# Performance work log

Measured on AMD Instinct MI355X. Metric: run time of the kernel, lower is better.

Reference implementation:

```python
import jax, jax.numpy as jnp
import numpy as np

K = 32          # init k
E = 0.003       # EMA rate e


def setup_inputs() -> dict:
    key = jax.random.key(0)
    k1, _ = jax.random.split(key)
    features = jax.random.normal(k1, (512, 6, 8192), dtype=jnp.float32)
    threshold = jnp.zeros((1,), dtype=jnp.float32)
    return {"features": features, "threshold": threshold}


def reference(features, threshold):
    batch_size, n_layers, d_features = features.shape
    batch_k = K * batch_size * n_layers
    flat = features.reshape(-1)                      # [B*L*D]
    topk_vals, topk_idxs = jax.lax.top_k(flat, batch_k)
    topk_vals = jax.nn.relu(topk_vals)
    out = jnp.zeros_like(flat).at[topk_idxs].set(topk_vals)
    out = out.reshape(batch_size, n_layers, d_features)
    min_k = jax.lax.stop_gradient(jnp.min(topk_vals))
    new_threshold = (1.0 - E) * threshold + E * min_k
    return out, new_threshold
```

## Files before the change

### kernel.cpp

```cpp
#include <hip/hip_runtime.h>
#include <stdint.h>

#define K_TOTAL   98304u
#define EMA_RATE  0.003f

#define SBINS      16384
#define SBIN_SHIFT 18
#define SAMPLE_VEC 131072
#define STARGET    8192u
#define P2_BINS    4096
#define P2_SHIFT   12
#define CAP2       65536u
#define EQCAP      256

#define MP_BLOCKS  1024
#define MP_THREADS 256
#define NWAVES     4096
#define WCAP       256
#define OCAP       65536u

__device__ __forceinline__ unsigned f2key(float x) {
    unsigned u = __float_as_uint(x);
    return (u & 0x80000000u) ? ~u : (u | 0x80000000u);
}
__device__ __forceinline__ float key2f(unsigned key) {
    unsigned u = (key & 0x80000000u) ? (key & 0x7FFFFFFFu) : ~key;
    return __uint_as_float(u);
}

__global__ __launch_bounds__(256) void sample_hist_kernel(
        const float4* __restrict__ in, unsigned* __restrict__ shist) {
    __shared__ unsigned h[SBINS];
    for (int i = threadIdx.x; i < SBINS; i += 256) h[i] = 0;
    __syncthreads();
    unsigned tid = blockIdx.x * 256 + threadIdx.x;
    unsigned nth = gridDim.x * 256;
    for (unsigned j = tid; j < SAMPLE_VEC; j += nth) {
        float4 v = in[j];
        atomicAdd(&h[f2key(v.x) >> SBIN_SHIFT], 1u);
        atomicAdd(&h[f2key(v.y) >> SBIN_SHIFT], 1u);
        atomicAdd(&h[f2key(v.z) >> SBIN_SHIFT], 1u);
        atomicAdd(&h[f2key(v.w) >> SBIN_SHIFT], 1u);
    }
    __syncthreads();
    for (int i = threadIdx.x; i < SBINS; i += 256) {
        unsigned c = h[i];
        if (c) atomicAdd(&shist[i], c);
    }
}

__global__ __launch_bounds__(1024) void sample_scan_kernel(
        const unsigned* __restrict__ shist, unsigned* __restrict__ res) {
    __shared__ unsigned psum[1024];
    const int T = 1024;
    const int GB = SBINS / T;
    int t = threadIdx.x;
    int hi = SBINS - 1 - t * GB;
    unsigned c[GB];
    #pragma unroll
    for (int j = 0; j < GB; ++j) c[j] = shist[hi - j];
    unsigned s = 0;
    #pragma unroll
    for (int j = 0; j < GB; ++j) s += c[j];
    psum[t] = s;
    __syncthreads();
    for (int off = 1; off < T; off <<= 1) {
        unsigned o = (t >= off) ? psum[t - off] : 0u;
        __syncthreads();
        psum[t] += o;
        __syncthreads();
    }
    unsigned cum = psum[t] - s;
    for (int j = 0; j < GB; ++j) {
        if (cum < STARGET && cum + c[j] >= STARGET) {
            unsigned bin = (unsigned)(hi - j);
            unsigned bb = (bin > 0) ? bin - 1 : 0;
            res[0] = bb << SBIN_SHIFT;
        }
        cum += c[j];
    }
}

__global__ __launch_bounds__(MP_THREADS) void main_pass_kernel(
        const float4* __restrict__ in, float4* __restrict__ out,
        const unsigned* __restrict__ res,
        uint2* __restrict__ wreg, unsigned* __restrict__ wcnt,
        uint2* __restrict__ ovf, unsigned* __restrict__ ocnt, int nvec) {
    unsigned tid  = blockIdx.x * MP_THREADS + threadIdx.x;
    unsigned nth  = gridDim.x * MP_THREADS;
    unsigned gw   = tid >> 6;
    unsigned lane = threadIdx.x & 63u;
    unsigned base = res[0];
    uint2* wb = wreg + (size_t)gw * WCAP;
    unsigned wcount = 0;
    const float4 z4 = make_float4(0.f, 0.f, 0.f, 0.f);
    for (unsigned i = tid; i < (unsigned)nvec; i += nth) {
        float4 v = in[i];
        out[i] = z4;
        unsigned idx = 4u * i;
        float xs[4] = {v.x, v.y, v.z, v.w};
        #pragma unroll
        for (int c = 0; c < 4; ++c) {
            unsigned key = f2key(xs[c]);
            bool pred = key >= base;
            unsigned long long mask = __ballot(pred);
            if (mask) {
                if (pred) {
                    unsigned prefix = __builtin_amdgcn_mbcnt_hi(
                        (unsigned)(mask >> 32),
                        __builtin_amdgcn_mbcnt_lo((unsigned)mask, 0u));
                    unsigned off = wcount + prefix;
                    if (off < WCAP) {
                        wb[off] = make_uint2(key, idx + c);
                    } else {
                        unsigned q = atomicAdd(ocnt, 1u);
                        if (q < OCAP) ovf[q] = make_uint2(key, idx + c);
                    }
                }
                wcount += (unsigned)__popcll(mask);
            }
        }
    }
    if (lane == 0) wcnt[gw] = (wcount < WCAP) ? wcount : WCAP;
}

__global__ __launch_bounds__(256) void cand_hist_kernel(
        const uint2* __restrict__ wreg, const unsigned* __restrict__ wcnt,
        const uint2* __restrict__ ovf, const unsigned* __restrict__ ocnt,
        const unsigned* __restrict__ res, unsigned* __restrict__ ghist) {
    __shared__ unsigned h[P2_BINS];
    for (int i = threadIdx.x; i < P2_BINS; i += 256) h[i] = 0;
    __syncthreads();
    unsigned base = res[0];
    unsigned tid = blockIdx.x * 256 + threadIdx.x;
    unsigned nth = gridDim.x * 256;
    const unsigned NSLOT = NWAVES * WCAP;
    for (unsigned s = tid; s < NSLOT; s += nth) {
        unsigned w = s >> 8, j = s & 255u;
        if (j < wcnt[w]) {
            unsigned g = (wreg[s].x - base) >> P2_SHIFT;
            if (g > P2_BINS - 1) g = P2_BINS - 1;
            atomicAdd(&h[g], 1u);
        }
    }
    unsigned no = min(*ocnt, OCAP);
    for (unsigned s = tid; s < no; s += nth) {
        unsigned g = (ovf[s].x - base) >> P2_SHIFT;
        if (g > P2_BINS - 1) g = P2_BINS - 1;
        atomicAdd(&h[g], 1u);
    }
    __syncthreads();
    for (int i = threadIdx.x; i < P2_BINS; i += 256) {
        unsigned c = h[i];
        if (c) atomicAdd(&ghist[i], c);
    }
}

__global__ __launch_bounds__(1024) void find_g_kernel(
        const unsigned* __restrict__ ghist, unsigned* __restrict__ res2) {
    __shared__ unsigned psum[1024];
    const int T = 1024;
    const int GB = P2_BINS / T;
    int t = threadIdx.x;
    int hi = P2_BINS - 1 - t * GB;
    unsigned c[GB];
    #pragma unroll
    for (int j = 0; j < GB; ++j) c[j] = ghist[hi - j];
    unsigned s = 0;
    #pragma unroll
    for (int j = 0; j < GB; ++j) s += c[j];
    psum[t] = s;
    __syncthreads();
    for (int off = 1; off < T; off <<= 1) {
        unsigned o = (t >= off) ? psum[t - off] : 0u;
        __syncthreads();
        psum[t] += o;
        __syncthreads();
    }
    unsigned cum = psum[t] - s;
    for (int j = 0; j < GB; ++j) {
        if (cum < K_TOTAL && cum + c[j] >= K_TOTAL) {
            res2[0] = (unsigned)(hi - j);
            res2[1] = K_TOTAL - cum;
        }
        cum += c[j];
    }
}

__global__ __launch_bounds__(256) void scatter_kernel(
        const uint2* __restrict__ wreg, const unsigned* __restrict__ wcnt,
        const uint2* __restrict__ ovf, const unsigned* __restrict__ ocnt,
        const unsigned* __restrict__ res, const unsigned* __restrict__ res2,
        unsigned* __restrict__ kval2, unsigned* __restrict__ cidx2,
        unsigned* __restrict__ cnt2, float* __restrict__ out) {
    unsigned base  = res[0];
    unsigned gstar = res2[0];
    unsigned tid = blockIdx.x * 256 + threadIdx.x;
    unsigned nth = gridDim.x * 256;
    const unsigned NSLOT = NWAVES * WCAP;
    for (unsigned s = tid; s < NSLOT; s += nth) {
        unsigned w = s >> 8, j = s & 255u;
        if (j < wcnt[w]) {
            uint2 e = wreg[s];
            unsigned g = (e.x - base) >> P2_SHIFT;
            if (g > P2_BINS - 1) g = P2_BINS - 1;
            if (g > gstar) {
                out[e.y] = fmaxf(key2f(e.x), 0.0f);
            } else if (g == gstar) {
                unsigned p = atomicAdd(cnt2, 1u);
                if (p < CAP2) { kval2[p] = e.x; cidx2[p] = e.y; }
            }
        }
    }
    unsigned no = min(*ocnt, OCAP);
    for (unsigned s = tid; s < no; s += nth) {
        uint2 e = ovf[s];
        unsigned g = (e.x - base) >> P2_SHIFT;
        if (g > P2_BINS - 1) g = P2_BINS - 1;
        if (g > gstar) {
            out[e.y] = fmaxf(key2f(e.x), 0.0f);
        } else if (g == gstar) {
            unsigned p = atomicAdd(cnt2, 1u);
            if (p < CAP2) { kval2[p] = e.x; cidx2[p] = e.y; }
        }
    }
}

__global__ __launch_bounds__(256) void final_kernel(
        const unsigned* __restrict__ kval2, const unsigned* __restrict__ cidx2,
        const unsigned* __restrict__ cnt2,
        const unsigned* __restrict__ res, const unsigned* __restrict__ res2,
        float* __restrict__ out,
        const float* __restrict__ thr_in, float* __restrict__ thr_out) {
    __shared__ unsigned h[1 << P2_SHIFT];
    __shared__ unsigned psum[256];
    __shared__ unsigned eqidx[EQCAP];
    __shared__ unsigned eqcnt;
    __shared__ unsigned sh_low, sh_need3;
    const int NB = 1 << P2_SHIFT;
    int t = threadIdx.x;
    unsigned nc2   = min(*cnt2, CAP2);
    unsigned base3 = res[0] + (res2[0] << P2_SHIFT);
    unsigned need2 = res2[1];

    for (int i = t; i < NB; i += 256) h[i] = 0;
    if (t == 0) eqcnt = 0;
    __syncthreads();
    for (unsigned i = t; i < nc2; i += 256) {
        unsigned low = kval2[i] - base3;
        if (low > (unsigned)(NB - 1)) low = NB - 1;
        atomicAdd(&h[low], 1u);
    }
    __syncthreads();

    const int GB = NB / 256;
    int hi = NB - 1 - t * GB;
    unsigned s = 0;
    for (int j = 0; j < GB; ++j) s += h[hi - j];
    psum[t] = s;
    __syncthreads();
    for (int off = 1; off < 256; off <<= 1) {
        unsigned o = (t >= off) ? psum[t - off] : 0u;
        __syncthreads();
        psum[t] += o;
        __syncthreads();
    }
    unsigned cum = psum[t] - s;
    for (int j = 0; j < GB; ++j) {
        unsigned c = h[hi - j];
        if (cum < need2 && cum + c >= need2) {
            sh_low = (unsigned)(hi - j);
            sh_need3 = need2 - cum;
        }
        cum += c;
    }
    __syncthreads();
    unsigned kth_key = base3 + sh_low;
    unsigned need3   = sh_need3;

    for (unsigned i = t; i < nc2; i += 256) {
        unsigned key = kval2[i];
        if (key > kth_key) {
            out[cidx2[i]] = fmaxf(key2f(key), 0.0f);
        } else if (key == kth_key) {
            unsigned p = atomicAdd(&eqcnt, 1u);
            if (p < EQCAP) eqidx[p] = cidx2[i];
        }
    }
    __syncthreads();

    unsigned ne = min(eqcnt, (unsigned)EQCAP);
    float vv = key2f(kth_key);
    for (unsigned e = t; e < ne; e += 256) {
        unsigned my = eqidx[e];
        unsigned rank = 0;
        for (unsigned f = 0; f < ne; ++f) rank += (eqidx[f] < my) ? 1u : 0u;
        if (rank < need3) out[my] = fmaxf(vv, 0.0f);
    }

    if (t == 0) {
        float mink = fmaxf(vv, 0.0f);
        thr_out[0] = (1.0f - EMA_RATE) * thr_in[0] + EMA_RATE * mink;
    }
}

extern "C" void kernel_launch(void* const* d_in, const int* in_sizes, int n_in,
                              void* d_out, int out_size, void* d_ws, size_t ws_size,
                              hipStream_t stream) {
    const float* feat   = (const float*)d_in[0];
    const float* thr_in = (const float*)d_in[1];
    float* out = (float*)d_out;
    int N    = in_sizes[0];
    int nvec = N / 4;

    uint8_t* w = (uint8_t*)d_ws;
    unsigned* shist = (unsigned*)w;
    unsigned* ghist = (unsigned*)(w + (64 << 10));
    unsigned* ctr   = (unsigned*)(w + (80 << 10));
    unsigned* ocnt  = ctr + 0;
    unsigned* cnt2  = ctr + 1;
    unsigned* res   = ctr + 4;
    unsigned* res2  = ctr + 8;
    unsigned* wcnt  = (unsigned*)(w + (84 << 10));

    uint2*    wreg  = (uint2*)(w + ((size_t)1 << 20));
    uint2*    ovf   = (uint2*)(w + ((size_t)9 << 20));
    unsigned* kval2 = (unsigned*)(w + ((size_t)10 << 20));
    unsigned* cidx2 = (unsigned*)(w + ((size_t)10 << 20) + CAP2 * 4);

    hipMemsetAsync(d_ws, 0, (84 << 10), stream);

    sample_hist_kernel<<<128, 256, 0, stream>>>((const float4*)feat, shist);
    sample_scan_kernel<<<1,  1024, 0, stream>>>(shist, res);
    main_pass_kernel  <<<MP_BLOCKS, MP_THREADS, 0, stream>>>(
        (const float4*)feat, (float4*)out, res, wreg, wcnt, ovf, ocnt, nvec);
    cand_hist_kernel  <<<128, 256, 0, stream>>>(wreg, wcnt, ovf, ocnt, res, ghist);
    find_g_kernel     <<<1,  1024, 0, stream>>>(ghist, res2);
    scatter_kernel    <<<128, 256, 0, stream>>>(wreg, wcnt, ovf, ocnt, res, res2,
                                                kval2, cidx2, cnt2, out);
    final_kernel      <<<1,   256, 0, stream>>>(kval2, cidx2, cnt2, res, res2,
                                                out, thr_in, out + N);
}
```

Before: 242.4 us.

## Fuse all top-k stages into one cooperative kernel with grid syncs

Replaces the memset and seven separate kernel launches with a single cooperative kernel that uses grid.sync between phases. The workspace is zeroed in-kernel, and the candidate histogram is built during the main pass, removing the separate re-read of candidate buffers. The sample is shrunk to fewer bins and elements, and the scatter phase gives each block its own wave region. This cuts launch and inter-kernel gaps but adds grid-wide barrier costs, needs all 1024 blocks co-resident, and uses a coarser sample threshold that could admit more candidates.

After: 785.6 us. 3.24x slower.

```diff
diff --git a/kernel.cpp b/kernel.cpp
--- a/kernel.cpp
+++ b/kernel.cpp
@@ -1,23 +1,28 @@
 #include <hip/hip_runtime.h>
+#include <hip/hip_cooperative_groups.h>
 #include <stdint.h>
+
+namespace cg = cooperative_groups;
 
 #define K_TOTAL   98304u
 #define EMA_RATE  0.003f
 
-#define SBINS      16384
-#define SBIN_SHIFT 18
-#define SAMPLE_VEC 131072
-#define STARGET    8192u
-#define P2_BINS    4096
-#define P2_SHIFT   12
-#define CAP2       65536u
-#define EQCAP      256
-
-#define MP_BLOCKS  1024
-#define MP_THREADS 256
-#define NWAVES     4096
-#define WCAP       256
-#define OCAP       65536u
+#define GRID_BLOCKS   1024
+#define BLOCK_THREADS 256
+#define NWAVES        4096
+#define WCAP          256
+
+#define SBINS         4096
+#define SSHIFT        20
+#define SAMPLE_V4     16384
+#define SAMPLE_BLOCKS 32
+#define STARGET       640u
+
+#define CBINS         4096
+#define CSHIFT        12
+#define CAP2          16384u
+#define OCAP          65536u
+#define EQCAP         256
 
 __device__ __forceinline__ unsigned f2key(float x) {
     unsigned u = __float_as_uint(x);
@@ -28,316 +33,287 @@
     return __uint_as_float(u);
 }
 
-__global__ __launch_bounds__(256) void sample_hist_kernel(
-        const float4* __restrict__ in, unsigned* __restrict__ shist) {
-    __shared__ unsigned h[SBINS];
-    for (int i = threadIdx.x; i < SBINS; i += 256) h[i] = 0;
-    __syncthreads();
-    unsigned tid = blockIdx.x * 256 + threadIdx.x;
-    unsigned nth = gridDim.x * 256;
-    for (unsigned j = tid; j < SAMPLE_VEC; j += nth) {
-        float4 v = in[j];
-        atomicAdd(&h[f2key(v.x) >> SBIN_SHIFT], 1u);
-        atomicAdd(&h[f2key(v.y) >> SBIN_SHIFT], 1u);
-        atomicAdd(&h[f2key(v.z) >> SBIN_SHIFT], 1u);
-        atomicAdd(&h[f2key(v.w) >> SBIN_SHIFT], 1u);
-    }
-    __syncthreads();
-    for (int i = threadIdx.x; i < SBINS; i += 256) {
-        unsigned c = h[i];
-        if (c) atomicAdd(&shist[i], c);
-    }
-}
-
-__global__ __launch_bounds__(1024) void sample_scan_kernel(
-        const unsigned* __restrict__ shist, unsigned* __restrict__ res) {
-    __shared__ unsigned psum[1024];
-    const int T = 1024;
-    const int GB = SBINS / T;
-    int t = threadIdx.x;
-    int hi = SBINS - 1 - t * GB;
-    unsigned c[GB];
-    #pragma unroll
-    for (int j = 0; j < GB; ++j) c[j] = shist[hi - j];
-    unsigned s = 0;
-    #pragma unroll
-    for (int j = 0; j < GB; ++j) s += c[j];
-    psum[t] = s;
-    __syncthreads();
-    for (int off = 1; off < T; off <<= 1) {
-        unsigned o = (t >= off) ? psum[t - off] : 0u;
-        __syncthreads();
-        psum[t] += o;
-        __syncthreads();
-    }
-    unsigned cum = psum[t] - s;
-    for (int j = 0; j < GB; ++j) {
-        if (cum < STARGET && cum + c[j] >= STARGET) {
-            unsigned bin = (unsigned)(hi - j);
-            unsigned bb = (bin > 0) ? bin - 1 : 0;
-            res[0] = bb << SBIN_SHIFT;
-        }
-        cum += c[j];
-    }
-}
-
-__global__ __launch_bounds__(MP_THREADS) void main_pass_kernel(
-        const float4* __restrict__ in, float4* __restrict__ out,
-        const unsigned* __restrict__ res,
-        uint2* __restrict__ wreg, unsigned* __restrict__ wcnt,
-        uint2* __restrict__ ovf, unsigned* __restrict__ ocnt, int nvec) {
-    unsigned tid  = blockIdx.x * MP_THREADS + threadIdx.x;
-    unsigned nth  = gridDim.x * MP_THREADS;
-    unsigned gw   = tid >> 6;
-    unsigned lane = threadIdx.x & 63u;
-    unsigned base = res[0];
-    uint2* wb = wreg + (size_t)gw * WCAP;
-    unsigned wcount = 0;
-    const float4 z4 = make_float4(0.f, 0.f, 0.f, 0.f);
-    for (unsigned i = tid; i < (unsigned)nvec; i += nth) {
-        float4 v = in[i];
-        out[i] = z4;
-        unsigned idx = 4u * i;
-        float xs[4] = {v.x, v.y, v.z, v.w};
-        #pragma unroll
-        for (int c = 0; c < 4; ++c) {
-            unsigned key = f2key(xs[c]);
-            bool pred = key >= base;
-            unsigned long long mask = __ballot(pred);
-            if (mask) {
-                if (pred) {
-                    unsigned prefix = __builtin_amdgcn_mbcnt_hi(
-                        (unsigned)(mask >> 32),
-                        __builtin_amdgcn_mbcnt_lo((unsigned)mask, 0u));
-                    unsigned off = wcount + prefix;
-                    if (off < WCAP) {
-                        wb[off] = make_uint2(key, idx + c);
-                    } else {
-                        unsigned q = atomicAdd(ocnt, 1u);
-                        if (q < OCAP) ovf[q] = make_uint2(key, idx + c);
-                    }
-                }
-                wcount += (unsigned)__popcll(mask);
-            }
-        }
-    }
-    if (lane == 0) wcnt[gw] = (wcount < WCAP) ? wcount : WCAP;
-}
-
-__global__ __launch_bounds__(256) void cand_hist_kernel(
-        const uint2* __restrict__ wreg, const unsigned* __restrict__ wcnt,
-        const uint2* __restrict__ ovf, const unsigned* __restrict__ ocnt,
-        const unsigned* __restrict__ res, unsigned* __restrict__ ghist) {
-    __shared__ unsigned h[P2_BINS];
-    for (int i = threadIdx.x; i < P2_BINS; i += 256) h[i] = 0;
-    __syncthreads();
-    unsigned base = res[0];
-    unsigned tid = blockIdx.x * 256 + threadIdx.x;
-    unsigned nth = gridDim.x * 256;
-    const unsigned NSLOT = NWAVES * WCAP;
-    for (unsigned s = tid; s < NSLOT; s += nth) {
-        unsigned w = s >> 8, j = s & 255u;
-        if (j < wcnt[w]) {
-            unsigned g = (wreg[s].x - base) >> P2_SHIFT;
-            if (g > P2_BINS - 1) g = P2_BINS - 1;
-            atomicAdd(&h[g], 1u);
-        }
-    }
-    unsigned no = min(*ocnt, OCAP);
-    for (unsigned s = tid; s < no; s += nth) {
-        unsigned g = (ovf[s].x - base) >> P2_SHIFT;
-        if (g > P2_BINS - 1) g = P2_BINS - 1;
-        atomicAdd(&h[g], 1u);
-    }
-    __syncthreads();
-    for (int i = threadIdx.x; i < P2_BINS; i += 256) {
-        unsigned c = h[i];
-        if (c) atomicAdd(&ghist[i], c);
-    }
-}
-
-__global__ __launch_bounds__(1024) void find_g_kernel(
-        const unsigned* __restrict__ ghist, unsigned* __restrict__ res2) {
-    __shared__ unsigned psum[1024];
-    const int T = 1024;
-    const int GB = P2_BINS / T;
-    int t = threadIdx.x;
-    int hi = P2_BINS - 1 - t * GB;
-    unsigned c[GB];
-    #pragma unroll
-    for (int j = 0; j < GB; ++j) c[j] = ghist[hi - j];
-    unsigned s = 0;
-    #pragma unroll
-    for (int j = 0; j < GB; ++j) s += c[j];
-    psum[t] = s;
-    __syncthreads();
-    for (int off = 1; off < T; off <<= 1) {
-        unsigned o = (t >= off) ? psum[t - off] : 0u;
-        __syncthreads();
-        psum[t] += o;
-        __syncthreads();
-    }
-    unsigned cum = psum[t] - s;
-    for (int j = 0; j < GB; ++j) {
-        if (cum < K_TOTAL && cum + c[j] >= K_TOTAL) {
-            res2[0] = (unsigned)(hi - j);
-            res2[1] = K_TOTAL - cum;
-        }
-        cum += c[j];
-    }
-}
-
-__global__ __launch_bounds__(256) void scatter_kernel(
-        const uint2* __restrict__ wreg, const unsigned* __restrict__ wcnt,
-        const uint2* __restrict__ ovf, const unsigned* __restrict__ ocnt,
-        const unsigned* __restrict__ res, const unsigned* __restrict__ res2,
+__global__ __launch_bounds__(BLOCK_THREADS) void topk_all(
+        const float4* __restrict__ in, float4* __restrict__ out4,
+        float* __restrict__ out,
+        unsigned* __restrict__ shist, unsigned* __restrict__ ghist,
+        unsigned* __restrict__ ctrs,  unsigned* __restrict__ wcnt,
+        uint2* __restrict__ wreg,     uint2* __restrict__ ovf,
         unsigned* __restrict__ kval2, unsigned* __restrict__ cidx2,
-        unsigned* __restrict__ cnt2, float* __restrict__ out) {
-    unsigned base  = res[0];
-    unsigned gstar = res2[0];
-    unsigned tid = blockIdx.x * 256 + threadIdx.x;
-    unsigned nth = gridDim.x * 256;
-    const unsigned NSLOT = NWAVES * WCAP;
-    for (unsigned s = tid; s < NSLOT; s += nth) {
-        unsigned w = s >> 8, j = s & 255u;
-        if (j < wcnt[w]) {
-            uint2 e = wreg[s];
-            unsigned g = (e.x - base) >> P2_SHIFT;
-            if (g > P2_BINS - 1) g = P2_BINS - 1;
-            if (g > gstar) {
-                out[e.y] = fmaxf(key2f(e.x), 0.0f);
-            } else if (g == gstar) {
-                unsigned p = atomicAdd(cnt2, 1u);
-                if (p < CAP2) { kval2[p] = e.x; cidx2[p] = e.y; }
-            }
-        }
-    }
-    unsigned no = min(*ocnt, OCAP);
-    for (unsigned s = tid; s < no; s += nth) {
-        uint2 e = ovf[s];
-        unsigned g = (e.x - base) >> P2_SHIFT;
-        if (g > P2_BINS - 1) g = P2_BINS - 1;
-        if (g > gstar) {
-            out[e.y] = fmaxf(key2f(e.x), 0.0f);
-        } else if (g == gstar) {
-            unsigned p = atomicAdd(cnt2, 1u);
-            if (p < CAP2) { kval2[p] = e.x; cidx2[p] = e.y; }
-        }
-    }
-}
-
-__global__ __launch_bounds__(256) void final_kernel(
-        const unsigned* __restrict__ kval2, const unsigned* __restrict__ cidx2,
-        const unsigned* __restrict__ cnt2,
-        const unsigned* __restrict__ res, const unsigned* __restrict__ res2,
-        float* __restrict__ out,
-        const float* __restrict__ thr_in, float* __restrict__ thr_out) {
-    __shared__ unsigned h[1 << P2_SHIFT];
-    __shared__ unsigned psum[256];
+        const float* __restrict__ thr_in, int nvec)
+{
+    cg::grid_group grid = cg::this_grid();
+    __shared__ unsigned h[CBINS];
+    __shared__ unsigned psum[BLOCK_THREADS];
     __shared__ unsigned eqidx[EQCAP];
     __shared__ unsigned eqcnt;
     __shared__ unsigned sh_low, sh_need3;
-    const int NB = 1 << P2_SHIFT;
-    int t = threadIdx.x;
-    unsigned nc2   = min(*cnt2, CAP2);
-    unsigned base3 = res[0] + (res2[0] << P2_SHIFT);
-    unsigned need2 = res2[1];
-
-    for (int i = t; i < NB; i += 256) h[i] = 0;
-    if (t == 0) eqcnt = 0;
-    __syncthreads();
-    for (unsigned i = t; i < nc2; i += 256) {
-        unsigned low = kval2[i] - base3;
-        if (low > (unsigned)(NB - 1)) low = NB - 1;
-        atomicAdd(&h[low], 1u);
-    }
-    __syncthreads();
-
-    const int GB = NB / 256;
-    int hi = NB - 1 - t * GB;
-    unsigned s = 0;
-    for (int j = 0; j < GB; ++j) s += h[hi - j];
-    psum[t] = s;
-    __syncthreads();
-    for (int off = 1; off < 256; off <<= 1) {
-        unsigned o = (t >= off) ? psum[t - off] : 0u;
-        __syncthreads();
-        psum[t] += o;
-        __syncthreads();
-    }
-    unsigned cum = psum[t] - s;
-    for (int j = 0; j < GB; ++j) {
-        unsigned c = h[hi - j];
-        if (cum < need2 && cum + c >= need2) {
-            sh_low = (unsigned)(hi - j);
-            sh_need3 = need2 - cum;
-        }
-        cum += c;
-    }
-    __syncthreads();
-    unsigned kth_key = base3 + sh_low;
-    unsigned need3   = sh_need3;
-
-    for (unsigned i = t; i < nc2; i += 256) {
-        unsigned key = kval2[i];
-        if (key > kth_key) {
-            out[cidx2[i]] = fmaxf(key2f(key), 0.0f);
-        } else if (key == kth_key) {
-            unsigned p = atomicAdd(&eqcnt, 1u);
-            if (p < EQCAP) eqidx[p] = cidx2[i];
-        }
-    }
-    __syncthreads();
-
-    unsigned ne = min(eqcnt, (unsigned)EQCAP);
-    float vv = key2f(kth_key);
-    for (unsigned e = t; e < ne; e += 256) {
-        unsigned my = eqidx[e];
-        unsigned rank = 0;
-        for (unsigned f = 0; f < ne; ++f) rank += (eqidx[f] < my) ? 1u : 0u;
-        if (rank < need3) out[my] = fmaxf(vv, 0.0f);
-    }
-
-    if (t == 0) {
-        float mink = fmaxf(vv, 0.0f);
-        thr_out[0] = (1.0f - EMA_RATE) * thr_in[0] + EMA_RATE * mink;
+
+    const unsigned t    = threadIdx.x;
+    const unsigned gtid = blockIdx.x * BLOCK_THREADS + t;
+
+    if (gtid < SBINS)                   shist[gtid] = 0;
+    else if (gtid < 2 * SBINS)          ghist[gtid - SBINS] = 0;
+    else if (gtid < 2 * SBINS + 8)      ctrs[gtid - 2 * SBINS] = 0;
+    grid.sync();
+
+    if (blockIdx.x < SAMPLE_BLOCKS) {
+        for (int i = t; i < SBINS; i += BLOCK_THREADS) h[i] = 0;
+        __syncthreads();
+        unsigned s0 = blockIdx.x * 512 + t;
+        #pragma unroll
+        for (int u = 0; u < 2; ++u) {
+            float4 v = in[s0 + u * 256];
+            atomicAdd(&h[f2key(v.x) >> SSHIFT], 1u);
+            atomicAdd(&h[f2key(v.y) >> SSHIFT], 1u);
+            atomicAdd(&h[f2key(v.z) >> SSHIFT], 1u);
+            atomicAdd(&h[f2key(v.w) >> SSHIFT], 1u);
+        }
+        __syncthreads();
+        for (int i = t; i < SBINS; i += BLOCK_THREADS) {
+            unsigned c = h[i];
+            if (c) atomicAdd(&shist[i], c);
+        }
+    }
+    grid.sync();
+
+    if (blockIdx.x == 0) {
+        const int GB = SBINS / BLOCK_THREADS;
+        int hi = SBINS - 1 - t * GB;
+        unsigned c[GB];
+        #pragma unroll
+        for (int j = 0; j < GB; ++j) c[j] = shist[hi - j];
+        unsigned s = 0;
+        #pragma unroll
+        for (int j = 0; j < GB; ++j) s += c[j];
+        psum[t] = s;
+        __syncthreads();
+        for (int off = 1; off < BLOCK_THREADS; off <<= 1) {
+            unsigned o = (t >= off) ? psum[t - off] : 0u;
+            __syncthreads();
+            psum[t] += o;
+            __syncthreads();
+        }
+        unsigned cum = psum[t] - s;
+        for (int j = 0; j < GB; ++j) {
+            if (cum < STARGET && cum + c[j] >= STARGET) {
+                unsigned bin = (unsigned)(hi - j);
+                unsigned bb = (bin > 0) ? bin - 1 : 0;
+                ctrs[2] = bb << SSHIFT;
+            }
+            cum += c[j];
+        }
+    }
+    grid.sync();
+
+    {
+        for (int i = t; i < CBINS; i += BLOCK_THREADS) h[i] = 0;
+        __syncthreads();
+        unsigned base = ctrs[2];
+        unsigned nth  = GRID_BLOCKS * BLOCK_THREADS;
+        unsigned gw   = gtid >> 6;
+        unsigned lane = t & 63u;
+        uint2* wb = wreg + (size_t)gw * WCAP;
+        unsigned wcount = 0;
+        const float4 z4 = make_float4(0.f, 0.f, 0.f, 0.f);
+        for (unsigned i = gtid; i < (unsigned)nvec; i += nth) {
+            float4 v = in[i];
+            out4[i] = z4;
+            unsigned idx = 4u * i;
+            float xs[4] = {v.x, v.y, v.z, v.w};
+            #pragma unroll
+            for (int c = 0; c < 4; ++c) {
+                unsigned key = f2key(xs[c]);
+                bool pred = key >= base;
+                unsigned long long mask = __ballot(pred);
+                if (mask) {
+                    if (pred) {
+                        unsigned prefix = __builtin_amdgcn_mbcnt_hi(
+                            (unsigned)(mask >> 32),
+                            __builtin_amdgcn_mbcnt_lo((unsigned)mask, 0u));
+                        unsigned off = wcount + prefix;
+                        unsigned g = (key - base) >> CSHIFT;
+                        if (g > CBINS - 1) g = CBINS - 1;
+                        atomicAdd(&h[g], 1u);
+                        if (off < WCAP) {
+                            wb[off] = make_uint2(key, idx + c);
+                        } else {
+                            unsigned q = atomicAdd(&ctrs[0], 1u);
+                            if (q < OCAP) ovf[q] = make_uint2(key, idx + c);
+                        }
+                    }
+                    wcount += (unsigned)__popcll(mask);
+                }
+            }
+        }
+        if (lane == 0) wcnt[gw] = (wcount < WCAP) ? wcount : WCAP;
+        __syncthreads();
+        for (int i = t; i < CBINS; i += BLOCK_THREADS) {
+            unsigned c = h[i];
+            if (c) atomicAdd(&ghist[i], c);
+        }
+    }
+    grid.sync();
+
+    if (blockIdx.x == 0) {
+        const int GB = CBINS / BLOCK_THREADS;
+        int hi = CBINS - 1 - t * GB;
+        unsigned c[GB];
+        #pragma unroll
+        for (int j = 0; j < GB; ++j) c[j] = ghist[hi - j];
+        unsigned s = 0;
+        #pragma unroll
+        for (int j = 0; j < GB; ++j) s += c[j];
+        psum[t] = s;
+        __syncthreads();
+        for (int off = 1; off < BLOCK_THREADS; off <<= 1) {
+            unsigned o = (t >= off) ? psum[t - off] : 0u;
+            __syncthreads();
+            psum[t] += o;
+            __syncthreads();
+        }
+        unsigned cum = psum[t] - s;
+        for (int j = 0; j < GB; ++j) {
+            if (cum < K_TOTAL && cum + c[j] >= K_TOTAL) {
+                ctrs[3] = (unsigned)(hi - j);
+                ctrs[4] = K_TOTAL - cum;
+            }
+            cum += c[j];
+        }
+    }
+    grid.sync();
+
+    {
+        unsigned base  = ctrs[2];
+        unsigned gstar = ctrs[3];
+        unsigned slot0 = blockIdx.x * 4 * WCAP;
+        for (unsigned j = t; j < 4 * WCAP; j += BLOCK_THREADS) {
+            unsigned w = (slot0 + j) >> 8;
+            if ((j & 255u) < wcnt[w]) {
+                uint2 e = wreg[slot0 + j];
+                unsigned g = (e.x - base) >> CSHIFT;
+                if (g > CBINS - 1) g = CBINS - 1;
+                if (g > gstar) {
+                    out[e.y] = fmaxf(key2f(e.x), 0.0f);
+                } else if (g == gstar) {
+                    unsigned p = atomicAdd(&ctrs[1], 1u);
+                    if (p < CAP2) { kval2[p] = e.x; cidx2[p] = e.y; }
+                }
+            }
+        }
+        if (blockIdx.x == 0) {
+            unsigned no = min(ctrs[0], (unsigned)OCAP);
+            for (unsigned s = t; s < no; s += BLOCK_THREADS) {
+                uint2 e = ovf[s];
+                unsigned g = (e.x - base) >> CSHIFT;
+                if (g > CBINS - 1) g = CBINS - 1;
+                if (g > gstar) {
+                    out[e.y] = fmaxf(key2f(e.x), 0.0f);
+                } else if (g == gstar) {
+                    unsigned p = atomicAdd(&ctrs[1], 1u);
+                    if (p < CAP2) { kval2[p] = e.x; cidx2[p] = e.y; }
+                }
+            }
+        }
+    }
+    grid.sync();
+
+    if (blockIdx.x == 0) {
+        unsigned nc2   = min(ctrs[1], (unsigned)CAP2);
+        unsigned base3 = ctrs[2] + (ctrs[3] << CSHIFT);
+        unsigned need2 = ctrs[4];
+        const int NB = 1 << CSHIFT;
+
+        for (int i = t; i < NB; i += BLOCK_THREADS) h[i] = 0;
+        if (t == 0) eqcnt = 0;
+        __syncthreads();
+        for (unsigned i = t; i < nc2; i += BLOCK_THREADS) {
+            unsigned low = kval2[i] - base3;
+            if (low > (unsigned)(NB - 1)) low = NB - 1;
+            atomicAdd(&h[low], 1u);
+        }
+        __syncthreads();
+
+        const int GB = NB / BLOCK_THREADS;
+        int hi = NB - 1 - t * GB;
+        unsigned s = 0;
+        for (int j = 0; j < GB; ++j) s += h[hi - j];
+        psum[t] = s;
+        __syncthreads();
+        for (int off = 1; off < BLOCK_THREADS; off <<= 1) {
+            unsigned o = (t >= off) ? psum[t - off] : 0u;
+            __syncthreads();
+            psum[t] += o;
+            __syncthreads();
+        }
+        unsigned cum = psum[t] - s;
+        for (int j = 0; j < GB; ++j) {
+            unsigned c = h[hi - j];
+            if (cum < need2 && cum + c >= need2) {
+                sh_low = (unsigned)(hi - j);
+                sh_need3 = need2 - cum;
+            }
+            cum += c;
+        }
+        __syncthreads();
+        unsigned kth_key = base3 + sh_low;
+        unsigned need3   = sh_need3;
+
+        for (unsigned i = t; i < nc2; i += BLOCK_THREADS) {
+            unsigned key = kval2[i];
+            if (key > kth_key) {
+                out[cidx2[i]] = fmaxf(key2f(key), 0.0f);
+            } else if (key == kth_key) {
+                unsigned p = atomicAdd(&eqcnt, 1u);
+                if (p < EQCAP) eqidx[p] = cidx2[i];
+            }
+        }
+        __syncthreads();
+
+        unsigned ne = min(eqcnt, (unsigned)EQCAP);
+        float vv = key2f(kth_key);
+        for (unsigned e = t; e < ne; e += BLOCK_THREADS) {
+            unsigned my = eqidx[e];
+            unsigned rank = 0;
+            for (unsigned f = 0; f < ne; ++f) rank += (eqidx[f] < my) ? 1u : 0u;
+            if (rank < need3) out[my] = fmaxf(vv, 0.0f);
+        }
+
+        if (t == 0) {
+            float mink = fmaxf(vv, 0.0f);
+            out[4 * (size_t)nvec] =
+                (1.0f - EMA_RATE) * thr_in[0] + EMA_RATE * mink;
+        }
     }
 }
 
 extern "C" void kernel_launch(void* const* d_in, const int* in_sizes, int n_in,
                               void* d_out, int out_size, void* d_ws, size_t ws_size,
                               hipStream_t stream) {
-    const float* feat   = (const float*)d_in[0];
-    const float* thr_in = (const float*)d_in[1];
-    float* out = (float*)d_out;
+    const float4* feat   = (const float4*)d_in[0];
+    const float*  thr_in = (const float*)d_in[1];
+    float*  out  = (float*)d_out;
+    float4* out4 = (float4*)d_out;
     int N    = in_sizes[0];
     int nvec = N / 4;
 
     uint8_t* w = (uint8_t*)d_ws;
     unsigned* shist = (unsigned*)w;
-    unsigned* ghist = (unsigned*)(w + (64 << 10));
-    unsigned* ctr   = (unsigned*)(w + (80 << 10));
-    unsigned* ocnt  = ctr + 0;
-    unsigned* cnt2  = ctr + 1;
-    unsigned* res   = ctr + 4;
-    unsigned* res2  = ctr + 8;
-    unsigned* wcnt  = (unsigned*)(w + (84 << 10));
-
+    unsigned* ghist = (unsigned*)(w + (16 << 10));
+    unsigned* ctrs  = (unsigned*)(w + (32 << 10));
+    unsigned* wcnt  = (unsigned*)(w + (36 << 10));
     uint2*    wreg  = (uint2*)(w + ((size_t)1 << 20));
-    uint2*    ovf   = (uint2*)(w + ((size_t)9 << 20));
-    unsigned* kval2 = (unsigned*)(w + ((size_t)10 << 20));
-    unsigned* cidx2 = (unsigned*)(w + ((size_t)10 << 20) + CAP2 * 4);
-
-    hipMemsetAsync(d_ws, 0, (84 << 10), stream);
-
-    sample_hist_kernel<<<128, 256, 0, stream>>>((const float4*)feat, shist);
-    sample_scan_kernel<<<1,  1024, 0, stream>>>(shist, res);
-    main_pass_kernel  <<<MP_BLOCKS, MP_THREADS, 0, stream>>>(
-        (const float4*)feat, (float4*)out, res, wreg, wcnt, ovf, ocnt, nvec);
-    cand_hist_kernel  <<<128, 256, 0, stream>>>(wreg, wcnt, ovf, ocnt, res, ghist);
-    find_g_kernel     <<<1,  1024, 0, stream>>>(ghist, res2);
-    scatter_kernel    <<<128, 256, 0, stream>>>(wreg, wcnt, ovf, ocnt, res, res2,
-                                                kval2, cidx2, cnt2, out);
-    final_kernel      <<<1,   256, 0, stream>>>(kval2, cidx2, cnt2, res, res2,
-                                                out, thr_in, out + N);
+    uint2*    ovf   = (uint2*)(w + ((size_t)10 << 20));
+    unsigned* kval2 = (unsigned*)(w + ((size_t)11 << 20));
+    unsigned* cidx2 = (unsigned*)(w + ((size_t)11 << 20) + CAP2 * 4);
+
+    void* args[] = {
+        (void*)&feat, (void*)&out4, (void*)&out,
+        (void*)&shist, (void*)&ghist, (void*)&ctrs, (void*)&wcnt,
+        (void*)&wreg, (void*)&ovf, (void*)&kval2, (void*)&cidx2,
+        (void*)&thr_in, (void*)&nvec
+    };
+    hipLaunchCooperativeKernel((void*)topk_all,
+                               dim3(GRID_BLOCKS), dim3(BLOCK_THREADS),
+                               args, 0, stream);
 }
```
